# Performance work log

Hardware: AMD Instinct MI355X
Metric: run time of the kernel (lower is better)

## Reference

```python
import jax, jax.numpy as jnp
import numpy as np

QMAX = 7.0      # symmetric int4 magnitude
GROUP = 64      # weight quant group size along input dim
RANK = 32       # SVD low-rank correction rank
EPS = 1e-8


def quantize_act(x):
    # per-token symmetric int4 fake-quant: scale = max|x| / 7 over feature dim
    s = jnp.maximum(jnp.max(jnp.abs(x), axis=-1, keepdims=True) / QMAX, EPS)
    q = jnp.clip(jnp.round(x / s), -8.0, 7.0)
    return q * s


def quantize_weight(w):
    # per-output-channel, per-group (GROUP along input dim) symmetric int4 fake-quant
    O, D = w.shape
    wg = w.reshape(O, D // GROUP, GROUP)
    s = jnp.maximum(jnp.max(jnp.abs(wg), axis=-1, keepdims=True) / QMAX, EPS)
    q = jnp.clip(jnp.round(wg / s), -8.0, 7.0)
    return (q * s).reshape(O, D)


def setup_inputs() -> dict:
    key = jax.random.key(0)
    k0, k1, k2, k3 = jax.random.split(key, 4)
    dim_in, dim_out2 = 3072, 24576
    x = jax.random.normal(k0, (1, 4096, dim_in), dtype=jnp.float32)
    w_res = jax.random.normal(k1, (dim_out2, dim_in), dtype=jnp.float32) * 0.02
    lora_down = jax.random.normal(k2, (RANK, dim_in), dtype=jnp.float32) * 0.02
    lora_up = jax.random.normal(k3, (dim_out2, RANK), dtype=jnp.float32) * 0.02
    return {"x": x, "w_res": w_res, "lora_down": lora_down, "lora_up": lora_up}


def reference(x, w_res, lora_down, lora_up):
    # SVDQW4A4Linear: quantized residual matmul + fp low-rank correction
    xq = quantize_act(x)                        # [B, S, D]
    wq = quantize_weight(w_res)                 # [O, D]
    out = jnp.einsum('bsd,od->bso', xq, wq)
    out = out + jnp.einsum('bsr,or->bso', jnp.einsum('bsd,rd->bsr', x, lora_down), lora_up)
    # GEGLU epilogue: chunk(2, dim=-1), x * gelu(gate)  (torch F.gelu = exact erf)
    h, gate = jnp.split(out, 2, axis=-1)
    return h * jax.nn.gelu(gate, approximate=False)
```

## Files before the change

### kernel.cpp

```cpp
#include <hip/hip_runtime.h>
#include <hip/hip_bf16.h>
#include <math.h>

typedef __bf16 bf16_t;
typedef __bf16 bf16x4 __attribute__((ext_vector_type(4)));
typedef __bf16 bf16x8 __attribute__((ext_vector_type(8)));
typedef float  f32x4  __attribute__((ext_vector_type(4)));

#define DIN   3072
#define NOUT  24576
#define HALF  12288
#define MTOK  4096
#define BM    128
#define BN    128
#define BK    64

#define NB_LORA  (MTOK / 8)
#define NB_QX    (MTOK)
#define NB_CVT   (NOUT * 32 / 4 / 256)
#define NB_QW    (NOUT * (DIN / 4) / 256)
#define B0       (NB_LORA)
#define B1       (B0 + NB_QX)
#define B2       (B1 + NB_CVT)
#define NB_PREP  (B2 + NB_QW)

#define GLD16(gp, lp) \
    __builtin_amdgcn_global_load_lds((const __attribute__((address_space(1))) void*)(gp), \
                                     (__attribute__((address_space(3))) void*)(lp), 16, 0, 0)

__global__ __launch_bounds__(256) void k_prep(const float* __restrict__ x,
                                              const float* __restrict__ w,
                                              const float* __restrict__ ld,
                                              const float* __restrict__ lu,
                                              bf16_t* __restrict__ xq,
                                              bf16_t* __restrict__ wq,
                                              bf16_t* __restrict__ T,
                                              bf16_t* __restrict__ lub) {
    const int bid = blockIdx.x;
    const int t = threadIdx.x;

    if (bid < B0) {
        int r = t & 31;
        int m = bid * 8 + (t >> 5);
        const float4* xr = reinterpret_cast<const float4*>(x + (size_t)m * DIN);
        const float4* lr = reinterpret_cast<const float4*>(ld + (size_t)r * DIN);
        float acc = 0.f;
#pragma unroll 4
        for (int i = 0; i < DIN / 4; ++i) {
            float4 a = xr[i], b = lr[i];
            acc += a.x * b.x + a.y * b.y + a.z * b.z + a.w * b.w;
        }
        T[(size_t)m * 32 + r] = (bf16_t)acc;
    } else if (bid < B1) {
        int m = bid - B0;
        const float4* row = reinterpret_cast<const float4*>(x + (size_t)m * DIN);
        float4 v[3];
        float vm = 0.f;
#pragma unroll
        for (int i = 0; i < 3; ++i) {
            v[i] = row[t + i * 256];
            vm = fmaxf(vm, fmaxf(fmaxf(fabsf(v[i].x), fabsf(v[i].y)),
                                 fmaxf(fabsf(v[i].z), fabsf(v[i].w))));
        }
#pragma unroll
        for (int d = 1; d < 64; d <<= 1) vm = fmaxf(vm, __shfl_xor(vm, d));
        __shared__ float sm[4];
        if ((t & 63) == 0) sm[t >> 6] = vm;
        __syncthreads();
        vm = fmaxf(fmaxf(sm[0], sm[1]), fmaxf(sm[2], sm[3]));
        float s = fmaxf(vm * (1.f / 7.f), 1e-8f);
        float inv = 1.f / s;
        bf16x4* orow = reinterpret_cast<bf16x4*>(xq + (size_t)m * DIN);
#pragma unroll
        for (int i = 0; i < 3; ++i) {
            bf16x4 o;
            o[0] = (bf16_t)(fminf(fmaxf(rintf(v[i].x * inv), -8.f), 7.f) * s);
            o[1] = (bf16_t)(fminf(fmaxf(rintf(v[i].y * inv), -8.f), 7.f) * s);
            o[2] = (bf16_t)(fminf(fmaxf(rintf(v[i].z * inv), -8.f), 7.f) * s);
            o[3] = (bf16_t)(fminf(fmaxf(rintf(v[i].w * inv), -8.f), 7.f) * s);
            orow[t + i * 256] = o;
        }
    } else if (bid < B2) {
        size_t idx = (size_t)(bid - B1) * 256 + t;
        float4 v = reinterpret_cast<const float4*>(lu)[idx];
        bf16x4 o;
        o[0] = (bf16_t)v.x; o[1] = (bf16_t)v.y; o[2] = (bf16_t)v.z; o[3] = (bf16_t)v.w;
        reinterpret_cast<bf16x4*>(lub)[idx] = o;
    } else {
        size_t idx = (size_t)(bid - B2) * 256 + t;
        f32x4 v = __builtin_nontemporal_load(reinterpret_cast<const f32x4*>(w) + idx);
        float vm = fmaxf(fmaxf(fabsf(v[0]), fabsf(v[1])), fmaxf(fabsf(v[2]), fabsf(v[3])));
        vm = fmaxf(vm, __shfl_xor(vm, 1));
        vm = fmaxf(vm, __shfl_xor(vm, 2));
        vm = fmaxf(vm, __shfl_xor(vm, 4));
        vm = fmaxf(vm, __shfl_xor(vm, 8));
        float s = fmaxf(vm * (1.f / 7.f), 1e-8f);
        float inv = 1.f / s;
        bf16x4 o;
        o[0] = (bf16_t)(fminf(fmaxf(rintf(v[0] * inv), -8.f), 7.f) * s);
        o[1] = (bf16_t)(fminf(fmaxf(rintf(v[1] * inv), -8.f), 7.f) * s);
        o[2] = (bf16_t)(fminf(fmaxf(rintf(v[2] * inv), -8.f), 7.f) * s);
        o[3] = (bf16_t)(fminf(fmaxf(rintf(v[3] * inv), -8.f), 7.f) * s);
        reinterpret_cast<bf16x4*>(wq)[idx] = o;
    }
}

__global__ __launch_bounds__(512, 2) void k_gemm(const bf16_t* __restrict__ xq,
                                                 const bf16_t* __restrict__ wq,
                                                 const bf16_t* __restrict__ T,
                                                 const bf16_t* __restrict__ lub,
                                                 float* __restrict__ out) {
    __shared__ __align__(16) char smem[65536];
    bf16_t* sA = (bf16_t*)smem;
    bf16_t* sH = sA + BM * BK;
    bf16_t* sG = sH + BN * BK;

    int tid = threadIdx.x, lane = tid & 63, w = tid >> 6;
    int half = w >> 2;
    int wr = (w & 3) >> 1, wc = w & 1;

    int nwg = gridDim.x;
    int cpx = nwg >> 3;
    int swz = (blockIdx.x & 7) * cpx + (blockIdx.x >> 3);
    int mt = swz & 31, nt = swz >> 5;
    int m0 = mt * BM, c0 = nt * BN;

    f32x4 acc[4][4];
#pragma unroll
    for (int i = 0; i < 4; ++i)
#pragma unroll
        for (int j = 0; j < 4; ++j) acc[i][j] = (f32x4){0.f, 0.f, 0.f, 0.f};

    const char* sBb = (const char*)(half ? sG : sH);
    const char* sAb = (const char*)sA;

    for (int k0 = 0; k0 < DIN; k0 += BK) {
        __syncthreads();
#pragma unroll
        for (int r = 0; r < 2; ++r) {
            int chunk = r * 512 + tid;
            int row = chunk >> 3;
            int gc = ((chunk & 7) ^ (row & 7)) * 8;
            int ldsoff = r * 4096 + w * 512;
            GLD16(xq + (size_t)(m0 + row) * DIN + k0 + gc, sA + ldsoff);
            GLD16(wq + (size_t)(c0 + row) * DIN + k0 + gc, sH + ldsoff);
            GLD16(wq + (size_t)(c0 + HALF + row) * DIN + k0 + gc, sG + ldsoff);
        }
        __syncthreads();

#pragma unroll
        for (int ks = 0; ks < 2; ++ks) {
            int c16 = ks * 4 + (lane >> 4);
            bf16x8 a[4], b[4];
#pragma unroll
            for (int i = 0; i < 4; ++i) {
                int ra = wr * 64 + i * 16 + (lane & 15);
                int rb = wc * 64 + i * 16 + (lane & 15);
                a[i] = *reinterpret_cast<const bf16x8*>(sAb + ra * 128 + ((c16 ^ (ra & 7)) << 4));
                b[i] = *reinterpret_cast<const bf16x8*>(sBb + rb * 128 + ((c16 ^ (rb & 7)) << 4));
            }
#pragma unroll
            for (int m = 0; m < 4; ++m)
#pragma unroll
                for (int n = 0; n < 4; ++n)
                    acc[m][n] = __builtin_amdgcn_mfma_f32_16x16x32_bf16(a[m], b[n], acc[m][n], 0, 0, 0);
        }
    }

    {
        bf16x8 tf[4];
#pragma unroll
        for (int m = 0; m < 4; ++m)
            tf[m] = *reinterpret_cast<const bf16x8*>(
                T + (size_t)(m0 + wr * 64 + m * 16 + (lane & 15)) * 32 + (lane >> 4) * 8);
#pragma unroll
        for (int n = 0; n < 4; ++n) {
            bf16x8 lu = *reinterpret_cast<const bf16x8*>(
                lub + (size_t)(c0 + half * HALF + wc * 64 + n * 16 + (lane & 15)) * 32 + (lane >> 4) * 8);
#pragma unroll
            for (int m = 0; m < 4; ++m)
                acc[m][n] = __builtin_amdgcn_mfma_f32_16x16x32_bf16(tf[m], lu, acc[m][n], 0, 0, 0);
        }
    }

    __syncthreads();
    float* exch = (float*)smem;
    if (half) {
#pragma unroll
        for (int m = 0; m < 4; ++m)
#pragma unroll
            for (int n = 0; n < 4; ++n) {
                int col = wc * 64 + n * 16 + (lane & 15);
#pragma unroll
                for (int r = 0; r < 4; ++r) {
                    int row = wr * 64 + m * 16 + (lane >> 4) * 4 + r;
                    float g = acc[m][n][r];
                    float gl = 0.5f * g * (1.0f + erff(g * 0.70710678118654752f));
                    exch[row * 128 + (col ^ (((row >> 2) & 3) << 4))] = gl;
                }
            }
    }
    __syncthreads();
    if (!half) {
#pragma unroll
        for (int m = 0; m < 4; ++m)
#pragma unroll
            for (int n = 0; n < 4; ++n) {
                int col = wc * 64 + n * 16 + (lane & 15);
#pragma unroll
                for (int r = 0; r < 4; ++r) {
                    int row = wr * 64 + m * 16 + (lane >> 4) * 4 + r;
                    int sidx = row * 128 + (col ^ (((row >> 2) & 3) << 4));
                    exch[sidx] = acc[m][n][r] * exch[sidx];
                }
            }
    }
    __syncthreads();
#pragma unroll
    for (int i = 0; i < 8; ++i) {
        int idx = i * 512 + tid;
        int row = idx >> 5;
        int c4 = idx & 31;
        f32x4 v = *reinterpret_cast<const f32x4*>(
            exch + row * 128 + ((c4 ^ (((row >> 2) & 3) << 2)) << 2));
        __builtin_nontemporal_store(v, reinterpret_cast<f32x4*>(
            out + (size_t)(m0 + row) * HALF + c0 + c4 * 4));
    }
}

extern "C" void kernel_launch(void* const* d_in, const int* in_sizes, int n_in,
                              void* d_out, int out_size, void* d_ws, size_t ws_size,
                              hipStream_t stream) {
    const float* x  = (const float*)d_in[0];
    const float* wr = (const float*)d_in[1];
    const float* ld = (const float*)d_in[2];
    const float* lu = (const float*)d_in[3];
    float* out = (float*)d_out;

    bf16_t* xq  = (bf16_t*)d_ws;
    bf16_t* wq  = xq + (size_t)MTOK * DIN;
    bf16_t* T   = wq + (size_t)NOUT * DIN;
    bf16_t* lub = T  + (size_t)MTOK * 32;

    k_prep<<<NB_PREP, 256, 0, stream>>>(x, wr, ld, lu, xq, wq, T, lub);
    k_gemm<<<(MTOK / BM) * (HALF / BN), 512, 0, stream>>>(xq, wq, T, lub, out);
}
```

Before: 755.3 us.

## Double-buffer GEMM LDS tiles with BN=96 and prefetch next K-slab

The GEMM main loop now double-buffers the A and B tiles in LDS. It issues global-to-LDS loads for the next K-slab before running the MFMAs on the current one, using one wait and barrier per iteration instead of two syncthreads. The output tile narrows from 128 to 96 columns per half, which raises the block count. It also precomputes LDS offsets and global pointers outside the loop and uses a padded rather than swizzled exchange layout in the epilogue. In exchange it uses 80KB of LDS, which limits occupancy, and each block gets a smaller MFMA tile with less reuse per load.

After: 782.9 us. +3.6%, slower.

```diff
diff --git a/kernel.cpp b/kernel.cpp
--- a/kernel.cpp
+++ b/kernel.cpp
@@ -12,8 +12,9 @@
 #define HALF  12288
 #define MTOK  4096
 #define BM    128
-#define BN    128
+#define BN    96
 #define BK    64
+#define NT    48
 
 #define NB_LORA  (MTOK / 8)
 #define NB_QX    (MTOK)
@@ -27,6 +28,10 @@
 #define GLD16(gp, lp) \
     __builtin_amdgcn_global_load_lds((const __attribute__((address_space(1))) void*)(gp), \
                                      (__attribute__((address_space(3))) void*)(lp), 16, 0, 0)
+
+#define BAR()    __builtin_amdgcn_s_barrier()
+#define WAITV(N) asm volatile("s_waitcnt vmcnt(" #N ")" ::: "memory")
+#define SCHED0() __builtin_amdgcn_sched_barrier(0)
 
 __global__ __launch_bounds__(256) void k_prep(const float* __restrict__ x,
                                               const float* __restrict__ w,
@@ -105,19 +110,17 @@
     }
 }
 
-__global__ __launch_bounds__(512, 2) void k_gemm(const bf16_t* __restrict__ xq,
+__global__ __launch_bounds__(512, 4) void k_gemm(const bf16_t* __restrict__ xq,
                                                  const bf16_t* __restrict__ wq,
                                                  const bf16_t* __restrict__ T,
                                                  const bf16_t* __restrict__ lub,
                                                  float* __restrict__ out) {
-    __shared__ __align__(16) char smem[65536];
-    bf16_t* sA = (bf16_t*)smem;
-    bf16_t* sH = sA + BM * BK;
-    bf16_t* sG = sH + BN * BK;
+    __shared__ __align__(16) char smem[81920];
 
     int tid = threadIdx.x, lane = tid & 63, w = tid >> 6;
     int half = w >> 2;
     int wr = (w & 3) >> 1, wc = w & 1;
+    const int l15 = lane & 15, lhi = lane >> 4;
 
     int nwg = gridDim.x;
     int cpx = nwg >> 3;
@@ -125,46 +128,93 @@
     int mt = swz & 31, nt = swz >> 5;
     int m0 = mt * BM, c0 = nt * BN;
 
-    f32x4 acc[4][4];
+    f32x4 acc[4][3];
 #pragma unroll
     for (int i = 0; i < 4; ++i)
 #pragma unroll
-        for (int j = 0; j < 4; ++j) acc[i][j] = (f32x4){0.f, 0.f, 0.f, 0.f};
-
-    const char* sBb = (const char*)(half ? sG : sH);
-    const char* sAb = (const char*)sA;
-
-    for (int k0 = 0; k0 < DIN; k0 += BK) {
-        __syncthreads();
-#pragma unroll
-        for (int r = 0; r < 2; ++r) {
-            int chunk = r * 512 + tid;
-            int row = chunk >> 3;
-            int gc = ((chunk & 7) ^ (row & 7)) * 8;
-            int ldsoff = r * 4096 + w * 512;
-            GLD16(xq + (size_t)(m0 + row) * DIN + k0 + gc, sA + ldsoff);
-            GLD16(wq + (size_t)(c0 + row) * DIN + k0 + gc, sH + ldsoff);
-            GLD16(wq + (size_t)(c0 + HALF + row) * DIN + k0 + gc, sG + ldsoff);
-        }
-        __syncthreads();
-
+        for (int j = 0; j < 3; ++j) acc[i][j] = (f32x4){0.f, 0.f, 0.f, 0.f};
+
+    const bf16_t* pS[5];
+    {
+        int ca0 = tid, ca1 = tid + 512;
+        int ra0 = ca0 >> 3, ra1 = ca1 >> 3;
+        pS[0] = xq + (size_t)(m0 + ra0) * DIN + ((ca0 & 7) ^ (ra0 & 7)) * 8;
+        pS[1] = xq + (size_t)(m0 + ra1) * DIN + ((ca1 & 7) ^ (ra1 & 7)) * 8;
+#pragma unroll
+        for (int j = 0; j < 3; ++j) {
+            int c = tid + j * 512;
+            int rs = c >> 3;
+            int grow = (rs < 96) ? (c0 + rs) : (c0 + HALF + rs - 96);
+            pS[2 + j] = wq + (size_t)grow * DIN + ((c & 7) ^ (rs & 7)) * 8;
+        }
+    }
+
+    int offA[4][2], offB[3][2];
+#pragma unroll
+    for (int ks = 0; ks < 2; ++ks) {
+        int c16 = ks * 4 + lhi;
+#pragma unroll
+        for (int i = 0; i < 4; ++i) {
+            int ra = wr * 64 + i * 16 + l15;
+            offA[i][ks] = ra * 128 + ((c16 ^ (ra & 7)) << 4);
+        }
+#pragma unroll
+        for (int n = 0; n < 3; ++n) {
+            int rb = half * 96 + wc * 48 + n * 16 + l15;
+            offB[n][ks] = rb * 128 + ((c16 ^ (rb & 7)) << 4);
+        }
+    }
+
+#define STAGE96(bA, bB)                                                       \
+    do {                                                                      \
+        GLD16(pS[0], (bA) + tid * 16);                                        \
+        GLD16(pS[1], (bA) + (tid + 512) * 16);                                \
+        GLD16(pS[2], (bB) + tid * 16);                                        \
+        GLD16(pS[3], (bB) + (tid + 512) * 16);                                \
+        GLD16(pS[4], (bB) + (tid + 1024) * 16);                               \
+    } while (0)
+
+    STAGE96((char*)smem, (char*)smem + 32768);
+#pragma unroll
+    for (int p = 0; p < 5; ++p) pS[p] += BK;
+    WAITV(0);
+    BAR();
+    SCHED0();
+
+    for (int t = 0; t < NT; ++t) {
+        const char* cA = (const char*)smem + (t & 1) * 16384;
+        const char* cB = (const char*)smem + 32768 + (t & 1) * 24576;
+        char* nA = (char*)smem + ((t + 1) & 1) * 16384;
+        char* nB = (char*)smem + 32768 + ((t + 1) & 1) * 24576;
+
+        STAGE96(nA, nB);
+
+        bf16x8 a[4][2], b[3][2];
 #pragma unroll
         for (int ks = 0; ks < 2; ++ks) {
-            int c16 = ks * 4 + (lane >> 4);
-            bf16x8 a[4], b[4];
-#pragma unroll
-            for (int i = 0; i < 4; ++i) {
-                int ra = wr * 64 + i * 16 + (lane & 15);
-                int rb = wc * 64 + i * 16 + (lane & 15);
-                a[i] = *reinterpret_cast<const bf16x8*>(sAb + ra * 128 + ((c16 ^ (ra & 7)) << 4));
-                b[i] = *reinterpret_cast<const bf16x8*>(sBb + rb * 128 + ((c16 ^ (rb & 7)) << 4));
-            }
-#pragma unroll
-            for (int m = 0; m < 4; ++m)
-#pragma unroll
-                for (int n = 0; n < 4; ++n)
-                    acc[m][n] = __builtin_amdgcn_mfma_f32_16x16x32_bf16(a[m], b[n], acc[m][n], 0, 0, 0);
-        }
+#pragma unroll
+            for (int i = 0; i < 4; ++i)
+                a[i][ks] = *reinterpret_cast<const bf16x8*>(cA + offA[i][ks]);
+#pragma unroll
+            for (int n = 0; n < 3; ++n)
+                b[n][ks] = *reinterpret_cast<const bf16x8*>(cB + offB[n][ks]);
+        }
+#pragma unroll
+        for (int m = 0; m < 4; ++m)
+#pragma unroll
+            for (int n = 0; n < 3; ++n)
+#pragma unroll
+                for (int ks = 0; ks < 2; ++ks)
+                    acc[m][n] = __builtin_amdgcn_mfma_f32_16x16x32_bf16(
+                        a[m][ks], b[n][ks], acc[m][n], 0, 0, 0);
+
+        WAITV(0);
+        BAR();
+        SCHED0();
+
+        const int adv = (t + 2 < NT) ? BK : 0;
+#pragma unroll
+        for (int p = 0; p < 5; ++p) pS[p] += adv;
     }
 
     {
@@ -172,11 +222,11 @@
 #pragma unroll
         for (int m = 0; m < 4; ++m)
             tf[m] = *reinterpret_cast<const bf16x8*>(
-                T + (size_t)(m0 + wr * 64 + m * 16 + (lane & 15)) * 32 + (lane >> 4) * 8);
-#pragma unroll
-        for (int n = 0; n < 4; ++n) {
+                T + (size_t)(m0 + wr * 64 + m * 16 + l15) * 32 + lhi * 8);
+#pragma unroll
+        for (int n = 0; n < 3; ++n) {
             bf16x8 lu = *reinterpret_cast<const bf16x8*>(
-                lub + (size_t)(c0 + half * HALF + wc * 64 + n * 16 + (lane & 15)) * 32 + (lane >> 4) * 8);
+                lub + (size_t)(c0 + half * HALF + wc * 48 + n * 16 + l15) * 32 + lhi * 8);
 #pragma unroll
             for (int m = 0; m < 4; ++m)
                 acc[m][n] = __builtin_amdgcn_mfma_f32_16x16x32_bf16(tf[m], lu, acc[m][n], 0, 0, 0);
@@ -189,14 +239,14 @@
 #pragma unroll
         for (int m = 0; m < 4; ++m)
 #pragma unroll
-            for (int n = 0; n < 4; ++n) {
-                int col = wc * 64 + n * 16 + (lane & 15);
+            for (int n = 0; n < 3; ++n) {
+                int col = wc * 48 + n * 16 + l15;
 #pragma unroll
                 for (int r = 0; r < 4; ++r) {
-                    int row = wr * 64 + m * 16 + (lane >> 4) * 4 + r;
+                    int row = wr * 64 + m * 16 + lhi * 4 + r;
                     float g = acc[m][n][r];
                     float gl = 0.5f * g * (1.0f + erff(g * 0.70710678118654752f));
-                    exch[row * 128 + (col ^ (((row >> 2) & 3) << 4))] = gl;
+                    exch[row * 100 + col] = gl;
                 }
             }
     }
@@ -205,27 +255,27 @@
 #pragma unroll
         for (int m = 0; m < 4; ++m)
 #pragma unroll
-            for (int n = 0; n < 4; ++n) {
-                int col = wc * 64 + n * 16 + (lane & 15);
+            for (int n = 0; n < 3; ++n) {
+                int col = wc * 48 + n * 16 + l15;
 #pragma unroll
                 for (int r = 0; r < 4; ++r) {
-                    int row = wr * 64 + m * 16 + (lane >> 4) * 4 + r;
-                    int sidx = row * 128 + (col ^ (((row >> 2) & 3) << 4));
+                    int row = wr * 64 + m * 16 + lhi * 4 + r;
+                    int sidx = row * 100 + col;
                     exch[sidx] = acc[m][n][r] * exch[sidx];
                 }
             }
     }
     __syncthreads();
 #pragma unroll
-    for (int i = 0; i < 8; ++i) {
+    for (int i = 0; i < 6; ++i) {
         int idx = i * 512 + tid;
-        int row = idx >> 5;
-        int c4 = idx & 31;
-        f32x4 v = *reinterpret_cast<const f32x4*>(
-            exch + row * 128 + ((c4 ^ (((row >> 2) & 3) << 2)) << 2));
+        int row = idx / 24;
+        int c4 = idx - row * 24;
+        f32x4 v = *reinterpret_cast<const f32x4*>(exch + row * 100 + c4 * 4);
         __builtin_nontemporal_store(v, reinterpret_cast<f32x4*>(
             out + (size_t)(m0 + row) * HALF + c0 + c4 * 4));
     }
+#undef STAGE96
 }
 
 extern "C" void kernel_launch(void* const* d_in, const int* in_sizes, int n_in,
```

## Double-buffer B tiles and prefetch next K-step during MFMA in GEMM loop

Applied to the files above, without the earlier changes.

The GEMM main loop becomes a software pipeline. The two weight tiles are double-buffered in a larger LDS allocation. The A tile is read into registers first, then its next slice is issued while the MFMAs run, with explicit vmcnt/lgkmcnt waits, raw barriers and sched barriers in place of __syncthreads. The aim is to hide global-to-LDS load latency behind compute. The launch bound is also raised to 4 blocks per CU, which tightens the per-thread register budget even though the 80KB LDS footprint still limits residency, so accumulator spills are a real risk.

Result: slower. 923.4 us (+22.2%).

```diff
diff --git a/kernel.cpp b/kernel.cpp
--- a/kernel.cpp
+++ b/kernel.cpp
@@ -14,6 +14,7 @@
 #define BM    128
 #define BN    128
 #define BK    64
+#define NT    48
 
 #define NB_LORA  (MTOK / 8)
 #define NB_QX    (MTOK)
@@ -27,6 +28,11 @@
 #define GLD16(gp, lp) \
     __builtin_amdgcn_global_load_lds((const __attribute__((address_space(1))) void*)(gp), \
                                      (__attribute__((address_space(3))) void*)(lp), 16, 0, 0)
+
+#define BAR()    __builtin_amdgcn_s_barrier()
+#define LGKM0()  asm volatile("s_waitcnt lgkmcnt(0)" ::: "memory")
+#define WAITV(N) asm volatile("s_waitcnt vmcnt(" #N ")" ::: "memory")
+#define SCHED0() __builtin_amdgcn_sched_barrier(0)
 
 __global__ __launch_bounds__(256) void k_prep(const float* __restrict__ x,
                                               const float* __restrict__ w,
@@ -105,19 +111,17 @@
     }
 }
 
-__global__ __launch_bounds__(512, 2) void k_gemm(const bf16_t* __restrict__ xq,
+__global__ __launch_bounds__(512, 4) void k_gemm(const bf16_t* __restrict__ xq,
                                                  const bf16_t* __restrict__ wq,
                                                  const bf16_t* __restrict__ T,
                                                  const bf16_t* __restrict__ lub,
                                                  float* __restrict__ out) {
-    __shared__ __align__(16) char smem[65536];
-    bf16_t* sA = (bf16_t*)smem;
-    bf16_t* sH = sA + BM * BK;
-    bf16_t* sG = sH + BN * BK;
+    __shared__ __align__(16) char smem[81920];
 
     int tid = threadIdx.x, lane = tid & 63, w = tid >> 6;
     int half = w >> 2;
     int wr = (w & 3) >> 1, wc = w & 1;
+    const int l15 = lane & 15, lhi = lane >> 4;
 
     int nwg = gridDim.x;
     int cpx = nwg >> 3;
@@ -131,40 +135,84 @@
 #pragma unroll
         for (int j = 0; j < 4; ++j) acc[i][j] = (f32x4){0.f, 0.f, 0.f, 0.f};
 
-    const char* sBb = (const char*)(half ? sG : sH);
-    const char* sAb = (const char*)sA;
-
-    for (int k0 = 0; k0 < DIN; k0 += BK) {
-        __syncthreads();
-#pragma unroll
-        for (int r = 0; r < 2; ++r) {
-            int chunk = r * 512 + tid;
-            int row = chunk >> 3;
-            int gc = ((chunk & 7) ^ (row & 7)) * 8;
-            int ldsoff = r * 4096 + w * 512;
-            GLD16(xq + (size_t)(m0 + row) * DIN + k0 + gc, sA + ldsoff);
-            GLD16(wq + (size_t)(c0 + row) * DIN + k0 + gc, sH + ldsoff);
-            GLD16(wq + (size_t)(c0 + HALF + row) * DIN + k0 + gc, sG + ldsoff);
-        }
-        __syncthreads();
-
+    const bf16_t *pA0, *pA1, *pH0, *pH1, *pG0, *pG1;
+    {
+        int c_lo = tid, c_hi = tid + 512;
+        int r_lo = c_lo >> 3, r_hi = c_hi >> 3;
+        int g_lo = ((c_lo & 7) ^ (r_lo & 7)) * 8;
+        int g_hi = ((c_hi & 7) ^ (r_hi & 7)) * 8;
+        pA0 = xq + (size_t)(m0 + r_lo) * DIN + g_lo;
+        pA1 = xq + (size_t)(m0 + r_hi) * DIN + g_hi;
+        pH0 = wq + (size_t)(c0 + r_lo) * DIN + g_lo;
+        pH1 = wq + (size_t)(c0 + r_hi) * DIN + g_hi;
+        pG0 = pH0 + (size_t)HALF * DIN;
+        pG1 = pH1 + (size_t)HALF * DIN;
+    }
+    char* const sA = (char*)smem;
+    const int dst_lo = tid * 16, dst_hi = (tid + 512) * 16;
+
+#define STAGE_B(nb)                                                           \
+    do {                                                                      \
+        GLD16(pH0, (nb) + dst_lo);         GLD16(pH1, (nb) + dst_hi);         \
+        GLD16(pG0, (nb) + 16384 + dst_lo); GLD16(pG1, (nb) + 16384 + dst_hi); \
+    } while (0)
+#define STAGE_A()                                                             \
+    do {                                                                      \
+        GLD16(pA0, sA + dst_lo);           GLD16(pA1, sA + dst_hi);           \
+    } while (0)
+
+    STAGE_A();
+    STAGE_B((char*)smem + 16384);
+    pA0 += BK; pA1 += BK; pH0 += BK; pH1 += BK; pG0 += BK; pG1 += BK;
+    WAITV(0);
+    BAR();
+    SCHED0();
+
+    for (int t = 0; t < NT; ++t) {
+        const char* cB = (const char*)smem + 16384 + (t & 1) * 32768;
+        char* nB = (char*)smem + 16384 + ((t + 1) & 1) * 32768;
+
+        STAGE_B(nB);
+
+        bf16x8 a[4][2];
 #pragma unroll
         for (int ks = 0; ks < 2; ++ks) {
-            int c16 = ks * 4 + (lane >> 4);
-            bf16x8 a[4], b[4];
+            int c16 = ks * 4 + lhi;
 #pragma unroll
             for (int i = 0; i < 4; ++i) {
-                int ra = wr * 64 + i * 16 + (lane & 15);
-                int rb = wc * 64 + i * 16 + (lane & 15);
-                a[i] = *reinterpret_cast<const bf16x8*>(sAb + ra * 128 + ((c16 ^ (ra & 7)) << 4));
-                b[i] = *reinterpret_cast<const bf16x8*>(sBb + rb * 128 + ((c16 ^ (rb & 7)) << 4));
+                int ra = wr * 64 + i * 16 + l15;
+                a[i][ks] = *reinterpret_cast<const bf16x8*>(sA + ra * 128 + ((c16 ^ (ra & 7)) << 4));
+            }
+        }
+        LGKM0();
+        BAR();
+        SCHED0();
+
+        STAGE_A();
+
+        const char* sB = cB + (half << 14);
+#pragma unroll
+        for (int ks = 0; ks < 2; ++ks) {
+            int c16 = ks * 4 + lhi;
+            bf16x8 b[4];
+#pragma unroll
+            for (int i = 0; i < 4; ++i) {
+                int rb = wc * 64 + i * 16 + l15;
+                b[i] = *reinterpret_cast<const bf16x8*>(sB + rb * 128 + ((c16 ^ (rb & 7)) << 4));
             }
 #pragma unroll
             for (int m = 0; m < 4; ++m)
 #pragma unroll
                 for (int n = 0; n < 4; ++n)
-                    acc[m][n] = __builtin_amdgcn_mfma_f32_16x16x32_bf16(a[m], b[n], acc[m][n], 0, 0, 0);
-        }
+                    acc[m][n] = __builtin_amdgcn_mfma_f32_16x16x32_bf16(a[m][ks], b[n], acc[m][n], 0, 0, 0);
+        }
+
+        WAITV(0);
+        BAR();
+        SCHED0();
+
+        const int adv = (t + 2 < NT) ? BK : 0;
+        pA0 += adv; pA1 += adv; pH0 += adv; pH1 += adv; pG0 += adv; pG1 += adv;
     }
 
     {
@@ -172,11 +220,11 @@
 #pragma unroll
         for (int m = 0; m < 4; ++m)
             tf[m] = *reinterpret_cast<const bf16x8*>(
-                T + (size_t)(m0 + wr * 64 + m * 16 + (lane & 15)) * 32 + (lane >> 4) * 8);
+                T + (size_t)(m0 + wr * 64 + m * 16 + l15) * 32 + lhi * 8);
 #pragma unroll
         for (int n = 0; n < 4; ++n) {
             bf16x8 lu = *reinterpret_cast<const bf16x8*>(
-                lub + (size_t)(c0 + half * HALF + wc * 64 + n * 16 + (lane & 15)) * 32 + (lane >> 4) * 8);
+                lub + (size_t)(c0 + half * HALF + wc * 64 + n * 16 + l15) * 32 + lhi * 8);
 #pragma unroll
             for (int m = 0; m < 4; ++m)
                 acc[m][n] = __builtin_amdgcn_mfma_f32_16x16x32_bf16(tf[m], lu, acc[m][n], 0, 0, 0);
@@ -190,10 +238,10 @@
         for (int m = 0; m < 4; ++m)
 #pragma unroll
             for (int n = 0; n < 4; ++n) {
-                int col = wc * 64 + n * 16 + (lane & 15);
+                int col = wc * 64 + n * 16 + l15;
 #pragma unroll
                 for (int r = 0; r < 4; ++r) {
-                    int row = wr * 64 + m * 16 + (lane >> 4) * 4 + r;
+                    int row = wr * 64 + m * 16 + lhi * 4 + r;
                     float g = acc[m][n][r];
                     float gl = 0.5f * g * (1.0f + erff(g * 0.70710678118654752f));
                     exch[row * 128 + (col ^ (((row >> 2) & 3) << 4))] = gl;
@@ -206,10 +254,10 @@
         for (int m = 0; m < 4; ++m)
 #pragma unroll
             for (int n = 0; n < 4; ++n) {
-                int col = wc * 64 + n * 16 + (lane & 15);
+                int col = wc * 64 + n * 16 + l15;
 #pragma unroll
                 for (int r = 0; r < 4; ++r) {
-                    int row = wr * 64 + m * 16 + (lane >> 4) * 4 + r;
+                    int row = wr * 64 + m * 16 + lhi * 4 + r;
                     int sidx = row * 128 + (col ^ (((row >> 2) & 3) << 4));
                     exch[sidx] = acc[m][n][r] * exch[sidx];
                 }
@@ -226,6 +274,8 @@
         __builtin_nontemporal_store(v, reinterpret_cast<f32x4*>(
             out + (size_t)(m0 + row) * HALF + c0 + c4 * 4));
     }
+#undef STAGE_B
+#undef STAGE_A
 }
 
 extern "C" void kernel_launch(void* const* d_in, const int* in_sizes, int n_in,
```
